# Kernel tuning notes

Measured on AMD Instinct MI355X. Metric: run time of the kernel, lower is better.

The kernel has to match this reference:

```python
import jax, jax.numpy as jnp
import numpy as np

N, M, D = 2048, 16, 256


def setup_inputs() -> dict:
    key = jax.random.key(0)
    k1, = jax.random.split(key, 1)
    embeddings = jax.random.normal(k1, (N, M, D), dtype=jnp.float32)
    w = jnp.asarray(10.0, dtype=jnp.float32)
    b = jnp.asarray(-5.0, dtype=jnp.float32)
    return {"embeddings": embeddings, "w": w, "b": b}


def reference(embeddings, w, b):
    # embeddings: [N, M, D]
    centroids = embeddings.mean(axis=1)          # [N, D]
    sum_ = embeddings.sum(axis=1)                # [N, D]
    e = embeddings.reshape(N * M, D)             # [NM, D]
    cosine_sim = e @ centroids.T                 # [NM, N]
    # excluded-self centroid for each (speaker j, utterance i):
    # cj = (sum_[j] - e_ji) / (M - 1); replace cosine_sim[ji, j] with dot(cj, e_ji)
    excl = (sum_[:, None, :] - embeddings) / (M - 1)           # [N, M, D]
    diag_vals = jnp.sum(excl * embeddings, axis=-1).reshape(N * M)  # [NM]
    labels = jnp.repeat(jnp.arange(N), M)                      # [NM]
    cosine_sim = cosine_sim.at[jnp.arange(N * M), labels].set(diag_vals)
    logits = w * cosine_sim + b                                # [NM, N]
    logp = jax.nn.log_softmax(logits, axis=-1)
    loss = -jnp.mean(logp[jnp.arange(N * M), labels])
    return loss
```

## Files before the change

### kernel.cpp

```cpp
#include <hip/hip_runtime.h>
#include <hip/hip_bf16.h>
#if !__has_builtin(__builtin_amdgcn_cvt_pk_fp8_f32)
#include <hip/hip_fp8.h>
#endif

#define NS 2048
#define MU 16
#define DD 256
#define NMROWS (NS*MU)
#define STRIPS 8
#define SC 256
#define NSTEP 4
#define BMROWS 128
#define THR 8.0f

typedef float  f32x4  __attribute__((ext_vector_type(4)));
typedef float  f32x16 __attribute__((ext_vector_type(16)));
typedef int    i32x4  __attribute__((ext_vector_type(4)));

#define LOG2E 1.44269504088896340736f
#define LN2   0.69314718055994530942f

#if __has_builtin(__builtin_amdgcn_exp2f)
#define EXP2F(x) __builtin_amdgcn_exp2f(x)
#else
#define EXP2F(x) exp2f(x)
#endif
#if __has_builtin(__builtin_amdgcn_logf)
#define LOG2F(x) __builtin_amdgcn_logf(x)
#else
#define LOG2F(x) __log2f(x)
#endif

__device__ __forceinline__ int pk4(float a, float b, float c, float d){
#if __has_builtin(__builtin_amdgcn_cvt_pk_fp8_f32)
  int v = __builtin_amdgcn_cvt_pk_fp8_f32(a, b, 0, false);
  v = __builtin_amdgcn_cvt_pk_fp8_f32(c, d, v, true);
  return v;
#else
  unsigned r = (unsigned)__hip_fp8_e4m3(a).__x
             | ((unsigned)__hip_fp8_e4m3(b).__x << 8)
             | ((unsigned)__hip_fp8_e4m3(c).__x << 16)
             | ((unsigned)__hip_fp8_e4m3(d).__x << 24);
  return (int)r;
#endif
}
__device__ __forceinline__ long mk64(int lo, int hi){
  return (long)(((unsigned long long)(unsigned)lo) |
                ((unsigned long long)(unsigned)hi << 32));
}


__launch_bounds__(256)
__global__ void prep_kernel(const float* __restrict__ emb,
                            const float* __restrict__ wp,
                            long* __restrict__ centk8,
                            unsigned char* __restrict__ embk8,
                            float* __restrict__ diag2){
  __shared__ float E[16*260];
  __shared__ float sm[256];
  const int t = threadIdx.x;
  const int n = blockIdx.x;
  const float* src = emb + (size_t)n*MU*DD;

  #pragma unroll
  for (int i=0;i<4;i++){
    int g = i*1024 + t*4;
    f32x4 v = *(const f32x4*)(src + g);
    int m = g >> 8, d = g & 255;
    *(f32x4*)&E[m*260 + d] = v;
  }
  __syncthreads();

  {
    float s = 0.f;
    #pragma unroll
    for (int m=0;m<16;m++) s += E[m*260 + t];
    sm[t] = s;
  }
  __syncthreads();

  const float w2 = wp[0] * LOG2E;

  if (t < 16){
    const float c16 = w2 * (1.0f/16.0f);
    const int st = t;
    const float* p = &sm[st*16];
    int q0 = pk4(p[0]*c16,  p[1]*c16,  p[2]*c16,  p[3]*c16);
    int q1 = pk4(p[4]*c16,  p[5]*c16,  p[6]*c16,  p[7]*c16);
    int q2 = pk4(p[8]*c16,  p[9]*c16,  p[10]*c16, p[11]*c16);
    int q3 = pk4(p[12]*c16, p[13]*c16, p[14]*c16, p[15]*c16);
    size_t base = ((size_t)(st*64 + (n>>5))*2)*32 + (n&31);
    centk8[base]      = mk64(q0, q1);
    centk8[base + 32] = mk64(q2, q3);
  }

  if (embk8){
    int st = t >> 4, r = t & 15;
    const float* p = &E[r*260 + st*16];
    i32x4 o;
    #pragma unroll
    for (int q=0;q<4;q++){
      f32x4 v = *(const f32x4*)(p + q*4);
      o[q] = pk4(v[0], v[1], v[2], v[3]);
    }
    *(i32x4*)(embk8 + ((size_t)st*NMROWS + n*16 + r)*16) = o;
  }

  {
    int m = t >> 4, j = t & 15;
    float acc = 0.f;
    #pragma unroll
    for (int i=0;i<16;i++){
      int d = j + 16*i;
      float e = E[m*260 + d];
      acc += e * (sm[d] - e);
    }
    acc += __shfl_xor(acc, 1, 16);
    acc += __shfl_xor(acc, 2, 16);
    acc += __shfl_xor(acc, 4, 16);
    acc += __shfl_xor(acc, 8, 16);
    if (j==0) diag2[n*16 + m] = acc * (w2 * (1.0f/15.0f));
  }
}

__device__ __forceinline__ void stage_b(const long* __restrict__ centk8,
                                        long* lds0, int cg0,
                                        int wave, int lane){
  #pragma unroll
  for (int i=0;i<4;i++){
    const int st = i*4 + wave;
    const long* g = centk8 + (size_t)(st*64 + cg0)*64 + lane*2;
    __builtin_amdgcn_global_load_lds(
        (const __attribute__((address_space(1))) void*)g,
        (__attribute__((address_space(3))) void*)(lds0 + (size_t)st*128),
        16, 0, 0);
  }
}

#define MFMA8(a,b,c) __builtin_amdgcn_mfma_f32_32x32x16_fp8_fp8(a,b,c,0,0,0)

template<bool FROMF32>
__launch_bounds__(256,4)
__global__ void ge2e_main(const float* __restrict__ embf,
                          const unsigned char* __restrict__ embk8,
                          const long* __restrict__ centk8,
                          const float* __restrict__ diag2,
                          float2* __restrict__ msbuf){
  __shared__ long Bbuf[2][2048];

  const int tid  = threadIdx.x;
  const int lane = tid & 63;
  const int wave = tid >> 6;
  const int l31  = lane & 31, hi = lane >> 5;
  const int strip  = blockIdx.x & 7;
  const int rowBlk = blockIdx.x >> 3;
  const int c0 = strip * SC;
  const int rowA = rowBlk*BMROWS + wave*32 + l31;

  stage_b(centk8, &Bbuf[0][0], c0 >> 5, wave, lane);

  long af[16];
  if constexpr (FROMF32){
    const float* rp = embf + (size_t)rowA*DD;
    #pragma unroll
    for (int st=0; st<16; ++st){
      f32x4 v0 = *(const f32x4*)(rp + 16*st + 8*hi);
      f32x4 v1 = *(const f32x4*)(rp + 16*st + 8*hi + 4);
      af[st] = mk64(pk4(v0[0],v0[1],v0[2],v0[3]), pk4(v1[0],v1[1],v1[2],v1[3]));
    }
  } else {
    #pragma unroll
    for (int st=0; st<16; ++st)
      af[st] = *(const long*)(embk8 + ((size_t)st*NMROWS + rowA)*16 + hi*8);
  }

  const float dv  = diag2[rowA];
  const int   lab = rowA >> 4;
  const int   labc0 = rowBlk*8;
  const bool  hasdiag = (labc0 >= c0) && (labc0 < c0 + SC);
  const int   dstep = (labc0 - c0) >> 6;
  const int   dgrp  = ((labc0 - c0) >> 5) & 1;

  float m = 0.f, s = 0.f;

  __syncthreads();

  for (int step=0; step<NSTEP; ++step){
    const int cb_ = step & 1;
    if (step+1 < NSTEP)
      stage_b(centk8, &Bbuf[cb_^1][0], (c0 >> 5) + (step+1)*2, wave, lane);

    const long* cur = &Bbuf[cb_][0];
    const int bi = hi*32 + l31;

    f32x16 accA, accB;
    #pragma unroll
    for (int i=0;i<16;i++){ accA[i] = 0.f; accB[i] = 0.f; }

    #pragma unroll
    for (int st=0; st<16; ++st){
      long b0 = cur[st*128 + bi];
      long b1 = cur[st*128 + 64 + bi];
      accA = MFMA8(b0, af[st], accA);
      accB = MFMA8(b1, af[st], accB);
    }

    if (hasdiag && step == dstep){
      int colbase = c0 + step*64 + dgrp*32 + 4*hi;
      if (dgrp == 0){
        #pragma unroll
        for (int r=0;r<16;r++){
          int col = colbase + (r&3) + 8*(r>>2);
          if (col == lab) accA[r] = dv;
        }
      } else {
        #pragma unroll
        for (int r=0;r<16;r++){
          int col = colbase + (r&3) + 8*(r>>2);
          if (col == lab) accB[r] = dv;
        }
      }
    }

    float xa0 = fmaxf(fmaxf(fmaxf(accA[0],accA[1]),fmaxf(accA[2],accA[3])),
                      fmaxf(fmaxf(accA[4],accA[5]),fmaxf(accA[6],accA[7])));
    float xa1 = fmaxf(fmaxf(fmaxf(accA[8],accA[9]),fmaxf(accA[10],accA[11])),
                      fmaxf(fmaxf(accA[12],accA[13]),fmaxf(accA[14],accA[15])));
    float xb0 = fmaxf(fmaxf(fmaxf(accB[0],accB[1]),fmaxf(accB[2],accB[3])),
                      fmaxf(fmaxf(accB[4],accB[5]),fmaxf(accB[6],accB[7])));
    float xb1 = fmaxf(fmaxf(fmaxf(accB[8],accB[9]),fmaxf(accB[10],accB[11])),
                      fmaxf(fmaxf(accB[12],accB[13]),fmaxf(accB[14],accB[15])));
    float tm = fmaxf(fmaxf(xa0,xa1), fmaxf(xb0,xb1));
    if (__any(tm > m + THR)){
      float mn = fmaxf(m, tm);
      s *= EXP2F(m - mn);
      m = mn;
    }
    float a0 = EXP2F(accA[0]-m)+EXP2F(accA[1]-m)+EXP2F(accA[2]-m)+EXP2F(accA[3]-m);
    float a1 = EXP2F(accA[4]-m)+EXP2F(accA[5]-m)+EXP2F(accA[6]-m)+EXP2F(accA[7]-m);
    float a2 = EXP2F(accA[8]-m)+EXP2F(accA[9]-m)+EXP2F(accA[10]-m)+EXP2F(accA[11]-m);
    float a3 = EXP2F(accA[12]-m)+EXP2F(accA[13]-m)+EXP2F(accA[14]-m)+EXP2F(accA[15]-m);
    float b0 = EXP2F(accB[0]-m)+EXP2F(accB[1]-m)+EXP2F(accB[2]-m)+EXP2F(accB[3]-m);
    float b1 = EXP2F(accB[4]-m)+EXP2F(accB[5]-m)+EXP2F(accB[6]-m)+EXP2F(accB[7]-m);
    float b2 = EXP2F(accB[8]-m)+EXP2F(accB[9]-m)+EXP2F(accB[10]-m)+EXP2F(accB[11]-m);
    float b3 = EXP2F(accB[12]-m)+EXP2F(accB[13]-m)+EXP2F(accB[14]-m)+EXP2F(accB[15]-m);
    s += ((a0+a1)+(a2+a3)) + ((b0+b1)+(b2+b3));

    asm volatile("s_waitcnt vmcnt(0)" ::: "memory");
    __builtin_amdgcn_s_barrier();
  }

  float mo = __shfl_xor(m,32,64), so = __shfl_xor(s,32,64);
  float mm = fmaxf(m,mo);
  float ss = s*EXP2F(m-mm) + so*EXP2F(mo-mm);

  if (hi==0) msbuf[(size_t)strip*NMROWS + rowA] = make_float2(mm, ss);
}

__launch_bounds__(512)
__global__ void merge_kernel(const float2* __restrict__ msbuf,
                             const float* __restrict__ diag2,
                             float* __restrict__ partials){
  __shared__ float sh[8];
  const int row = blockIdx.x*512 + threadIdx.x;
  float2 p[STRIPS];
  #pragma unroll
  for (int k=0;k<STRIPS;k++) p[k] = msbuf[(size_t)k*NMROWS + row];
  float mm = p[0].x;
  #pragma unroll
  for (int k=1;k<STRIPS;k++) mm = fmaxf(mm, p[k].x);
  float ss = 0.f;
  #pragma unroll
  for (int k=0;k<STRIPS;k++) ss += p[k].y * EXP2F(p[k].x - mm);
  float term = LN2*(mm + LOG2F(ss) - diag2[row]);
  #pragma unroll
  for (int off=32; off; off>>=1) term += __shfl_xor(term, off, 64);
  if ((threadIdx.x & 63)==0) sh[threadIdx.x>>6] = term;
  __syncthreads();
  if (threadIdx.x==0){
    float v = 0.f;
    #pragma unroll
    for (int i=0;i<8;i++) v += sh[i];
    partials[blockIdx.x] = v;
  }
}

__global__ void final_kernel(const float* __restrict__ partials,
                             float* __restrict__ out){
  int tid = threadIdx.x;
  float v = partials[tid];
  #pragma unroll
  for (int off=32; off; off>>=1) v += __shfl_xor(v, off, 64);
  if (tid==0) out[0] = v * (1.0f/NMROWS);
}

extern "C" void kernel_launch(void* const* d_in, const int* in_sizes, int n_in,
                              void* d_out, int out_size, void* d_ws, size_t ws_size,
                              hipStream_t stream){
  const float* emb = (const float*)d_in[0];
  const float* wp  = (const float*)d_in[1];
  float* out = (float*)d_out;
  char* ws = (char*)d_ws;

  const size_t centk_b = (size_t)NS*DD;
  const size_t embk_b  = (size_t)NMROWS*DD;
  const size_t diag_b  = (size_t)NMROWS*4;
  const size_t ms_b    = (size_t)STRIPS*NMROWS*8;
  const bool useEmbk = ws_size >= centk_b + embk_b + diag_b + ms_b + 1024;

  long* centk8 = (long*)ws;
  size_t off = centk_b;
  unsigned char* embk8 = useEmbk ? (unsigned char*)(ws + off) : nullptr;
  if (useEmbk) off += embk_b;
  float*  diag2 = (float*)(ws + off);  off += diag_b;
  float2* msbuf = (float2*)(ws + off); off += ms_b;
  float*  parts = (float*)(ws + off);

  prep_kernel<<<NS, 256, 0, stream>>>(emb, wp, centk8, embk8, diag2);
  if (useEmbk)
    ge2e_main<false><<<(NMROWS/BMROWS)*STRIPS, 256, 0, stream>>>(emb, embk8, centk8, diag2, msbuf);
  else
    ge2e_main<true><<<(NMROWS/BMROWS)*STRIPS, 256, 0, stream>>>(emb, embk8, centk8, diag2, msbuf);
  merge_kernel<<<NMROWS/512, 512, 0, stream>>>(msbuf, diag2, parts);
  final_kernel<<<1, 64, 0, stream>>>(parts, out);
}
```

Measured before the change: 47.35 us.

## Stage whole centroid strip in LDS once with 512-thread blocks and fold max offset into MFMA init

Blocks grow to 512 threads covering 256 rows and load the entire 256-column centroid strip into LDS up front (64KB). This removes the per-step double buffering, the waitcnt and the barriers. The running-max subtraction moves into the MFMA accumulator initialisation (starting from -m), which drops the per-element subtractions in the common exp path. The risks are higher LDS use per block, which limits occupancy, and a longer initial load before any compute can start.

Measured after the change: 50.86 us. +7.4%, slower.

```diff
diff --git a/kernel.cpp b/kernel.cpp
--- a/kernel.cpp
+++ b/kernel.cpp
@@ -11,7 +11,7 @@
 #define STRIPS 8
 #define SC 256
 #define NSTEP 4
-#define BMROWS 128
+#define BMROWS 256
 #define THR 8.0f
 
 typedef float  f32x4  __attribute__((ext_vector_type(4)));
@@ -124,16 +124,18 @@
   }
 }
 
-__device__ __forceinline__ void stage_b(const long* __restrict__ centk8,
-                                        long* lds0, int cg0,
-                                        int wave, int lane){
-  #pragma unroll
-  for (int i=0;i<4;i++){
-    const int st = i*4 + wave;
-    const long* g = centk8 + (size_t)(st*64 + cg0)*64 + lane*2;
+__device__ __forceinline__ void stage_strip(const long* __restrict__ centk8,
+                                            long* lds, int cg0,
+                                            int wave, int lane){
+  #pragma unroll
+  for (int i=0;i<8;i++){
+    const int L  = wave*8 + i;
+    const int st = L >> 2;
+    const int q  = L & 3;
+    const long* g = centk8 + (size_t)(st*64 + cg0)*64 + q*128 + lane*2;
     __builtin_amdgcn_global_load_lds(
         (const __attribute__((address_space(1))) void*)g,
-        (__attribute__((address_space(3))) void*)(lds0 + (size_t)st*128),
+        (__attribute__((address_space(3))) void*)(lds + (size_t)st*512 + q*128),
         16, 0, 0);
   }
 }
@@ -141,13 +143,13 @@
 #define MFMA8(a,b,c) __builtin_amdgcn_mfma_f32_32x32x16_fp8_fp8(a,b,c,0,0,0)
 
 template<bool FROMF32>
-__launch_bounds__(256,4)
+__launch_bounds__(512,4)
 __global__ void ge2e_main(const float* __restrict__ embf,
                           const unsigned char* __restrict__ embk8,
                           const long* __restrict__ centk8,
                           const float* __restrict__ diag2,
                           float2* __restrict__ msbuf){
-  __shared__ long Bbuf[2][2048];
+  __shared__ long Bs[8192];
 
   const int tid  = threadIdx.x;
   const int lane = tid & 63;
@@ -158,7 +160,7 @@
   const int c0 = strip * SC;
   const int rowA = rowBlk*BMROWS + wave*32 + l31;
 
-  stage_b(centk8, &Bbuf[0][0], c0 >> 5, wave, lane);
+  stage_strip(centk8, Bs, c0 >> 5, wave, lane);
 
   long af[16];
   if constexpr (FROMF32){
@@ -177,33 +179,34 @@
 
   const float dv  = diag2[rowA];
   const int   lab = rowA >> 4;
-  const int   labc0 = rowBlk*8;
+  const int   labc0 = rowBlk*16;
   const bool  hasdiag = (labc0 >= c0) && (labc0 < c0 + SC);
   const int   dstep = (labc0 - c0) >> 6;
   const int   dgrp  = ((labc0 - c0) >> 5) & 1;
 
-  float m = 0.f, s = 0.f;
+  float mneg = 0.f, s = 0.f;
 
   __syncthreads();
 
+  #pragma unroll
   for (int step=0; step<NSTEP; ++step){
-    const int cb_ = step & 1;
-    if (step+1 < NSTEP)
-      stage_b(centk8, &Bbuf[cb_^1][0], (c0 >> 5) + (step+1)*2, wave, lane);
-
-    const long* cur = &Bbuf[cb_][0];
-    const int bi = hi*32 + l31;
+    f32x16 ci;
+    #pragma unroll
+    for (int i=0;i<16;i++) ci[i] = mneg;
 
     f32x16 accA, accB;
-    #pragma unroll
-    for (int i=0;i<16;i++){ accA[i] = 0.f; accB[i] = 0.f; }
-
-    #pragma unroll
-    for (int st=0; st<16; ++st){
-      long b0 = cur[st*128 + bi];
-      long b1 = cur[st*128 + 64 + bi];
-      accA = MFMA8(b0, af[st], accA);
-      accB = MFMA8(b1, af[st], accB);
+    {
+      const long bA = Bs[(size_t)((0*8 + step*2    )*2 + hi)*32 + l31];
+      const long bB = Bs[(size_t)((0*8 + step*2 + 1)*2 + hi)*32 + l31];
+      accA = MFMA8(bA, af[0], ci);
+      accB = MFMA8(bB, af[0], ci);
+    }
+    #pragma unroll
+    for (int st=1; st<16; ++st){
+      const long bA = Bs[(size_t)((st*8 + step*2    )*2 + hi)*32 + l31];
+      const long bB = Bs[(size_t)((st*8 + step*2 + 1)*2 + hi)*32 + l31];
+      accA = MFMA8(bA, af[st], accA);
+      accB = MFMA8(bB, af[st], accB);
     }
 
     if (hasdiag && step == dstep){
@@ -212,13 +215,13 @@
         #pragma unroll
         for (int r=0;r<16;r++){
           int col = colbase + (r&3) + 8*(r>>2);
-          if (col == lab) accA[r] = dv;
+          if (col == lab) accA[r] = dv + mneg;
         }
       } else {
         #pragma unroll
         for (int r=0;r<16;r++){
           int col = colbase + (r&3) + 8*(r>>2);
-          if (col == lab) accB[r] = dv;
+          if (col == lab) accB[r] = dv + mneg;
         }
       }
     }
@@ -232,25 +235,29 @@
     float xb1 = fmaxf(fmaxf(fmaxf(accB[8],accB[9]),fmaxf(accB[10],accB[11])),
                       fmaxf(fmaxf(accB[12],accB[13]),fmaxf(accB[14],accB[15])));
     float tm = fmaxf(fmaxf(xa0,xa1), fmaxf(xb0,xb1));
-    if (__any(tm > m + THR)){
-      float mn = fmaxf(m, tm);
-      s *= EXP2F(m - mn);
-      m = mn;
-    }
-    float a0 = EXP2F(accA[0]-m)+EXP2F(accA[1]-m)+EXP2F(accA[2]-m)+EXP2F(accA[3]-m);
-    float a1 = EXP2F(accA[4]-m)+EXP2F(accA[5]-m)+EXP2F(accA[6]-m)+EXP2F(accA[7]-m);
-    float a2 = EXP2F(accA[8]-m)+EXP2F(accA[9]-m)+EXP2F(accA[10]-m)+EXP2F(accA[11]-m);
-    float a3 = EXP2F(accA[12]-m)+EXP2F(accA[13]-m)+EXP2F(accA[14]-m)+EXP2F(accA[15]-m);
-    float b0 = EXP2F(accB[0]-m)+EXP2F(accB[1]-m)+EXP2F(accB[2]-m)+EXP2F(accB[3]-m);
-    float b1 = EXP2F(accB[4]-m)+EXP2F(accB[5]-m)+EXP2F(accB[6]-m)+EXP2F(accB[7]-m);
-    float b2 = EXP2F(accB[8]-m)+EXP2F(accB[9]-m)+EXP2F(accB[10]-m)+EXP2F(accB[11]-m);
-    float b3 = EXP2F(accB[12]-m)+EXP2F(accB[13]-m)+EXP2F(accB[14]-m)+EXP2F(accB[15]-m);
-    s += ((a0+a1)+(a2+a3)) + ((b0+b1)+(b2+b3));
-
-    asm volatile("s_waitcnt vmcnt(0)" ::: "memory");
-    __builtin_amdgcn_s_barrier();
-  }
-
+
+    if (__any(tm > THR)){
+      float d = fmaxf(tm, 0.f);
+      s *= EXP2F(-d);
+      mneg -= d;
+      float a0=0.f, b0=0.f;
+      #pragma unroll
+      for (int r=0;r<16;r++){ a0 += EXP2F(accA[r]-d); b0 += EXP2F(accB[r]-d); }
+      s += a0 + b0;
+    } else {
+      float a0 = EXP2F(accA[0])+EXP2F(accA[1])+EXP2F(accA[2])+EXP2F(accA[3]);
+      float a1 = EXP2F(accA[4])+EXP2F(accA[5])+EXP2F(accA[6])+EXP2F(accA[7]);
+      float a2 = EXP2F(accA[8])+EXP2F(accA[9])+EXP2F(accA[10])+EXP2F(accA[11]);
+      float a3 = EXP2F(accA[12])+EXP2F(accA[13])+EXP2F(accA[14])+EXP2F(accA[15]);
+      float b0 = EXP2F(accB[0])+EXP2F(accB[1])+EXP2F(accB[2])+EXP2F(accB[3]);
+      float b1 = EXP2F(accB[4])+EXP2F(accB[5])+EXP2F(accB[6])+EXP2F(accB[7]);
+      float b2 = EXP2F(accB[8])+EXP2F(accB[9])+EXP2F(accB[10])+EXP2F(accB[11]);
+      float b3 = EXP2F(accB[12])+EXP2F(accB[13])+EXP2F(accB[14])+EXP2F(accB[15]);
+      s += ((a0+a1)+(a2+a3)) + ((b0+b1)+(b2+b3));
+    }
+  }
+
+  float m  = -mneg;
   float mo = __shfl_xor(m,32,64), so = __shfl_xor(s,32,64);
   float mm = fmaxf(m,mo);
   float ss = s*EXP2F(m-mm) + so*EXP2F(mo-mm);
@@ -319,9 +326,9 @@
 
   prep_kernel<<<NS, 256, 0, stream>>>(emb, wp, centk8, embk8, diag2);
   if (useEmbk)
-    ge2e_main<false><<<(NMROWS/BMROWS)*STRIPS, 256, 0, stream>>>(emb, embk8, centk8, diag2, msbuf);
+    ge2e_main<false><<<(NMROWS/BMROWS)*STRIPS, 512, 0, stream>>>(emb, embk8, centk8, diag2, msbuf);
   else
-    ge2e_main<true><<<(NMROWS/BMROWS)*STRIPS, 256, 0, stream>>>(emb, embk8, centk8, diag2, msbuf);
+    ge2e_main<true><<<(NMROWS/BMROWS)*STRIPS, 512, 0, stream>>>(emb, embk8, centk8, diag2, msbuf);
   merge_kernel<<<NMROWS/512, 512, 0, stream>>>(msbuf, diag2, parts);
   final_kernel<<<1, 64, 0, stream>>>(parts, out);
 }
```
